# Optimization experiments

Hardware: AMD Instinct MI355X
Metric: run time of the kernel (lower is better)

Reference implementation:

```python
import jax, jax.numpy as jnp
import numpy as np
from jax import lax

V = 50000          # vocab
E = 64             # embedding_dim
B = 64             # batch
SEQ = 1024         # sentence length
NC = 6             # num_classes
L = 4              # num_layers (total conv layers)
KTOP = 4
NF = [10, 14, 18, 22]          # num_filters per stage
KS = [7, 5, 5, 3]              # kernel sizes
ROWS = [E // 2**i for i in range(5)]   # [64,32,16,8,4]
GROUPS = ROWS[:4]              # conv_i groups = rows[i-1]
# dynamic k-max schedule: k_l = max(k_top, ceil((L-l)/L * SEQ)) for l=1,2,3; last pool uses k_top
KPOOL = [max(KTOP, int(np.ceil((L - l) / L * SEQ))) for l in (1, 2, 3)] + [KTOP]  # [768,512,256,4]


def _uniform(key, shape, fan):
    s = 1.0 / np.sqrt(fan)
    return jax.random.uniform(key, shape, jnp.float32, -s, s)


def setup_inputs() -> dict:
    key = jax.random.key(0)
    ks = jax.random.split(key, 16)
    tokens = jax.random.randint(ks[0], (B, SEQ), 0, V)
    emb = jax.random.normal(ks[1], (V, E), jnp.float32)
    inp = {"tokens": tokens, "emb": emb}
    # conv weights: OIH layout, I = in_channels / groups = num_filters[i-1] (or 1 for conv1)
    in_pg = [1, NF[0], NF[1], NF[2]]
    out_ch = [NF[i] * ROWS[i] for i in range(4)]   # [640,448,288,176]
    for i in range(4):
        fan = in_pg[i] * KS[i]
        inp[f"w{i+1}"] = _uniform(ks[2 + 2 * i], (out_ch[i], in_pg[i], KS[i]), fan)
        inp[f"b{i+1}"] = _uniform(ks[3 + 2 * i], (out_ch[i],), fan)
    fc_in = ROWS[4] * NF[3] * KTOP   # 4*22*4 = 352
    inp["fcw"] = _uniform(ks[10], (NC, fc_in), fc_in)
    inp["fcb"] = _uniform(ks[11], (NC,), fc_in)
    return inp


def _fold(x, nf):
    # channel index c = row*nf + filt; sum adjacent rows pairwise (Fold(2,2))
    b, d, s = x.shape
    r = d // nf
    return x.reshape(b, r // 2, 2, nf, s).sum(axis=2).reshape(b, d // 2, s)


def _kmax(x, k):
    # top-k along seq axis, preserving original temporal order
    _, idx = lax.top_k(x, k)
    idx = jnp.sort(idx, axis=-1)
    return jnp.take_along_axis(x, idx, axis=-1)


def reference(tokens, emb, w1, b1, w2, b2, w3, b3, w4, b4, fcw, fcb):
    x = emb[tokens]                 # (B, S, E)
    x = x.transpose(0, 2, 1)        # (B, E, S)
    ws, bs = (w1, w2, w3, w4), (b1, b2, b3, b4)
    for i in range(4):
        pad = KS[i] - 1             # 'wide' convolution
        x = lax.conv_general_dilated(
            x, ws[i], (1,), [(pad, pad)],
            dimension_numbers=("NCH", "OIH", "NCH"),
            feature_group_count=GROUPS[i],
        ) + bs[i][None, :, None]
        x = _fold(x, NF[i])
        x = _kmax(x, KPOOL[i])
        x = jnp.tanh(x)
    # dropout is identity in eval mode
    x = x.reshape(x.shape[0], -1)   # (B, 352)
    return x @ fcw.T + fcb
```

## Files before the change

### kernel.cpp

```cpp
#include <hip/hip_runtime.h>
#include <hip/hip_bf16.h>
#include <math.h>


#if defined(__has_builtin)
#if __has_builtin(__builtin_amdgcn_ballot_w64)
#define BALLOT64(expr) __builtin_amdgcn_ballot_w64(expr)
#endif
#endif
#ifndef BALLOT64
#define BALLOT64(expr) __ballot(expr)
#endif

__device__ __forceinline__ unsigned f2ord(float f) {
    unsigned u = __float_as_uint(f);
    return (u & 0x80000000u) ? ~u : (u | 0x80000000u);
}
__device__ __forceinline__ float ord2f(unsigned key) {
    unsigned u = (key & 0x80000000u) ? (key & 0x7fffffffu) : ~key;
    return __uint_as_float(u);
}
__device__ __forceinline__ float tanh_fast(float x) {
    float e = __expf(2.f * x);
    return 1.f - 2.f * __builtin_amdgcn_rcpf(e + 1.f);
}
__device__ __forceinline__ int mbcnt64(unsigned long long m) {
    return __builtin_amdgcn_mbcnt_hi((unsigned)(m >> 32),
           __builtin_amdgcn_mbcnt_lo((unsigned)m, 0u));
}

template<int CH>
__device__ __forceinline__ int count_ge(const unsigned* keys, unsigned t) {
    int c = 0;
    #pragma unroll
    for (int i = 0; i < CH; ++i)
        c += __popcll(BALLOT64((keys[i] >= t)));
    return c;
}

template<int CH>
__device__ __forceinline__ void select_finish(const unsigned* keys, unsigned T,
                                              int k, float* stage,
                                              float* __restrict__ out)
{
    int g = 0, e = 0;
    #pragma unroll
    for (int i = 0; i < CH; ++i) { g += (keys[i] > T); e += (keys[i] == T); }

    int gtBefore = 0, eqBefore = 0, totG = 0;
    #pragma unroll
    for (int b = 0; b < 5; ++b) {
        unsigned long long mg = BALLOT64((((g >> b) & 1) != 0));
        unsigned long long me = BALLOT64((((e >> b) & 1) != 0));
        gtBefore += mbcnt64(mg) << b;
        eqBefore += mbcnt64(me) << b;
        totG     += __popcll(mg) << b;
    }
    const int needTies = k - totG;

    int gRun = 0, eRun = 0;
    #pragma unroll
    for (int i = 0; i < CH; ++i) {
        const unsigned key = keys[i];
        const bool isG = key > T;
        const bool isE = key == T;
        const int eIdx = eqBefore + eRun;
        const int dst = gtBefore + gRun + min(eIdx, needTies);
        if (isG || (isE && eIdx < needTies))
            stage[dst] = tanh_fast(ord2f(key));
        gRun += isG; eRun += isE;
    }
    const int lane = threadIdx.x & 63;
    float4* o4 = (float4*)out;
    const float4* s4 = (const float4*)stage;
    for (int i = lane; i < (k >> 2); i += 64)
        o4[i] = s4[i];
}

template<int N, int CH, int RADIX>
__device__ void wave_selectN(const unsigned (*keys)[CH], int k, float* stage,
                             float* const* outs)
{
    unsigned p[N];
    int above[N], buck[N];
    #pragma unroll
    for (int n = 0; n < N; ++n) { p[n] = 0u; above[n] = 0; buck[n] = 64 * CH; }

    unsigned doneMask = 0;
    const unsigned allDone = (1u << N) - 1u;

    if (RADIX == 4) {
        #pragma unroll 1
        for (int pos = 15; pos >= 0; --pos) {
            #pragma unroll
            for (int n = 0; n < N; ++n) {
                if (!((doneMask >> n) & 1u)) {
                    const int sh = 2 * pos;
                    const unsigned t1 = p[n] | (1u << sh);
                    const unsigned t2 = p[n] | (2u << sh);
                    const unsigned t3 = p[n] | (3u << sh);
                    const int c1 = count_ge<CH>(keys[n], t1);
                    const int c2 = count_ge<CH>(keys[n], t2);
                    const int c3 = count_ge<CH>(keys[n], t3);
                    const int rem = k - above[n];
                    if (c3 - above[n] >= rem) {
                        p[n] = t3; buck[n] = c3 - above[n];
                    } else if (c2 - above[n] >= rem) {
                        p[n] = t2; buck[n] = c2 - c3; above[n] = c3;
                    } else if (c1 - above[n] >= rem) {
                        p[n] = t1; buck[n] = c1 - c2; above[n] = c2;
                    } else {
                        buck[n] -= (c1 - above[n]); above[n] = c1;
                    }
                    if (buck[n] == k - above[n]) doneMask |= (1u << n);
                }
            }
            if (doneMask == allDone) break;
        }
    } else {
        #pragma unroll 1
        for (int pos = 31; pos >= 0; --pos) {
            #pragma unroll
            for (int n = 0; n < N; ++n) {
                if (!((doneMask >> n) & 1u)) {
                    const unsigned t = p[n] | (1u << pos);
                    const int c = count_ge<CH>(keys[n], t);
                    const int inb = c - above[n];
                    const int rem = k - above[n];
                    if (inb >= rem) { p[n] = t; buck[n] = inb; }
                    else            { above[n] += inb; buck[n] -= inb; }
                    if (buck[n] == k - above[n]) doneMask |= (1u << n);
                }
            }
            if (doneMask == allDone) break;
        }
    }
    #pragma unroll
    for (int n = 0; n < N; ++n)
        select_finish<CH>(keys[n], p[n], k, stage, outs[n]);
}

__global__ __launch_bounds__(128) void layer1_fused(
    const int* __restrict__ tokens, const float* __restrict__ emb,
    const float* __restrict__ W1, const float* __restrict__ B1,
    float* __restrict__ Z1)
{
    const int j = blockIdx.x;
    const int b = blockIdx.y;
    const int t = threadIdx.x;
    const int w = t >> 6;
    const int lane = t & 63;

    __shared__ float xr[2][1100];
    __shared__ __align__(16) float stagebuf[2][768];

    const float2* emb2 = (const float2*)emb;
    for (int i = t; i < 1100; i += 128) {
        int s = i - 6;
        float a = 0.f, c = 0.f;
        if (s >= 0 && s < 1024) {
            int tok = tokens[b * 1024 + s];
            float2 v = emb2[(size_t)tok * 32 + j];
            a = v.x; c = v.y;
        }
        xr[0][i] = a;
        xr[1][i] = c;
    }
    __syncthreads();

    const int beg = lane * 17;

    float x0[23], x1[23];
    #pragma unroll
    for (int i = 0; i < 23; ++i) { x0[i] = xr[0][beg + i]; x1[i] = xr[1][beg + i]; }

    unsigned keys[5][17];
    float* outs[5];
    const size_t orow = (size_t)b * 320 + (size_t)j * 10;

    #pragma unroll
    for (int q = 0; q < 5; ++q) {
        const int f = 5 * w + q;
        float wa[7], wb[7];
        #pragma unroll
        for (int k2 = 0; k2 < 7; ++k2) {
            wa[k2] = W1[(2 * j * 10 + f) * 7 + k2];
            wb[k2] = W1[((2 * j + 1) * 10 + f) * 7 + k2];
        }
        const float bias = B1[2 * j * 10 + f] + B1[(2 * j + 1) * 10 + f];
        #pragma unroll
        for (int i = 0; i < 17; ++i) {
            float acc = bias;
            #pragma unroll
            for (int k2 = 0; k2 < 7; ++k2)
                acc += x0[i + k2] * wa[k2] + x1[i + k2] * wb[k2];
            keys[q][i] = (beg + i < 1030) ? f2ord(acc) : 0u;
        }
        outs[q] = Z1 + (orow + f) * 768;
    }
    wave_selectN<5, 17, 4>(keys, 768, stagebuf[w], outs);
}

template <int IPG, int NF, int K, int SIN, int SOUT, int KSEL, int NW, int CH,
          int PHASES>
__global__ __launch_bounds__(NW * 64) void conv_fold_select_kernel(
    const float* __restrict__ X, const float* __restrict__ W,
    const float* __restrict__ Bias, float* __restrict__ Z,
    int Cin, int Cfold)
{
    static_assert(NF == 2 * NW, "2 filters per wave");
    static_assert(64 * CH >= SOUT, "chunk covers row");
    constexpr int W2 = 64 * CH + K - 1;
    constexpr int RS = 2 * IPG / PHASES;

    const int t = threadIdx.x;
    const int j = blockIdx.x;
    const int b = blockIdx.y;
    const int wav = t >> 6, lane = t & 63;

    __shared__ float xs[RS][W2];
    __shared__ __align__(16) float stagebuf[NW][KSEL];

    const float* Xb = X + ((size_t)b * Cin + (size_t)(2 * j) * IPG) * SIN;

    const int f0 = __builtin_amdgcn_readfirstlane(2 * wav);
    float acc0[CH], acc1[CH];
    {
        float bias0 = Bias[2 * j * NF + f0]     + Bias[(2 * j + 1) * NF + f0];
        float bias1 = Bias[2 * j * NF + f0 + 1] + Bias[(2 * j + 1) * NF + f0 + 1];
        #pragma unroll
        for (int i = 0; i < CH; ++i) { acc0[i] = bias0; acc1[i] = bias1; }
    }
    const int base = lane * CH;

    #pragma unroll 1
    for (int ph = 0; ph < PHASES; ++ph) {
        if (ph) __syncthreads();
        for (int idx = t; idx < RS * W2; idx += NW * 64) {
            int r = idx / W2, p = idx - r * W2;
            int sg = p - (K - 1);
            int gr = ph * RS + r;
            xs[r][p] = (sg >= 0 && sg < SIN) ? Xb[(size_t)gr * SIN + sg] : 0.f;
        }
        __syncthreads();

        int h = (ph * RS) / IPG, c = (ph * RS) % IPG;
        #pragma unroll 1
        for (int r = 0; r < RS; ++r) {
            float win[CH + K - 1];
            #pragma unroll
            for (int p = 0; p < CH + K - 1; ++p)
                win[p] = xs[r][base + p];
            const float* Wp = W + ((size_t)((2 * j + h) * NF + f0) * IPG + c) * K;
            #pragma unroll
            for (int k2 = 0; k2 < K; ++k2) {
                const float w0 = Wp[k2];
                const float w1 = Wp[(size_t)IPG * K + k2];
                #pragma unroll
                for (int i = 0; i < CH; ++i) {
                    acc0[i] = fmaf(win[i + k2], w0, acc0[i]);
                    acc1[i] = fmaf(win[i + k2], w1, acc1[i]);
                }
            }
            if (++c == IPG) { c = 0; ++h; }
        }
    }

    unsigned keys[2][CH];
    #pragma unroll
    for (int i = 0; i < CH; ++i) {
        keys[0][i] = (base + i < SOUT) ? f2ord(acc0[i]) : 0u;
        keys[1][i] = (base + i < SOUT) ? f2ord(acc1[i]) : 0u;
    }
    const size_t orow = (size_t)b * Cfold + (size_t)j * NF;
    float* outs[2] = { Z + (orow + f0) * (size_t)KSEL,
                       Z + (orow + f0 + 1) * (size_t)KSEL };
    wave_selectN<2, CH, 2>(keys, KSEL, stagebuf[wav], outs);
}

__global__ __launch_bounds__(192) void fc_kernel(
    const float* __restrict__ Z, const float* __restrict__ Wf,
    const float* __restrict__ bf, float* __restrict__ out)
{
    int g = blockIdx.x * blockDim.x + threadIdx.x;
    if (g >= 64 * 6) return;
    int b = g / 6, c = g % 6;
    float acc = bf[c];
    const float* zr = Z + b * 352;
    const float* wr = Wf + c * 352;
    for (int i = 0; i < 352; ++i) acc += zr[i] * wr[i];
    out[g] = acc;
}

extern "C" void kernel_launch(void* const* d_in, const int* in_sizes, int n_in,
                              void* d_out, int out_size, void* d_ws, size_t ws_size,
                              hipStream_t stream)
{
    const int*   tokens = (const int*)  d_in[0];
    const float* emb    = (const float*)d_in[1];
    const float* w1     = (const float*)d_in[2];
    const float* b1     = (const float*)d_in[3];
    const float* w2     = (const float*)d_in[4];
    const float* b2     = (const float*)d_in[5];
    const float* w3     = (const float*)d_in[6];
    const float* b3     = (const float*)d_in[7];
    const float* w4     = (const float*)d_in[8];
    const float* b4     = (const float*)d_in[9];
    const float* fcw    = (const float*)d_in[10];
    const float* fcb    = (const float*)d_in[11];
    float* out = (float*)d_out;
    float* ws  = (float*)d_ws;

    float* Z1 = ws;
    float* Z2 = ws + 15728640;
    float* Z3 = ws;
    float* Z4 = ws + 2359296;

    layer1_fused<<<dim3(32, 64), 128, 0, stream>>>(tokens, emb, w1, b1, Z1);

    conv_fold_select_kernel<10, 14, 5, 768, 772, 512, 7, 13, 2>
        <<<dim3(16, 64), 7 * 64, 0, stream>>>(Z1, w2, b2, Z2, 320, 224);

    conv_fold_select_kernel<14, 18, 5, 512, 516, 256, 9, 9, 1>
        <<<dim3(8, 64), 9 * 64, 0, stream>>>(Z2, w3, b3, Z3, 224, 144);

    conv_fold_select_kernel<18, 22, 3, 256, 258, 4, 11, 5, 1>
        <<<dim3(4, 64), 11 * 64, 0, stream>>>(Z3, w4, b4, Z4, 144, 88);

    fc_kernel<<<2, 192, 0, stream>>>(Z4, fcw, fcb, out);
}
```

Measured before the change: 345.8 us.

## Fuse layers 1-2 and 3-4 into kernels keeping intermediates in LDS

Merges the layer-1 conv+fold+k-max with the layer-2 conv so Z1 stays in shared memory and never goes to global memory. Likewise merges layers 3 and 4 so Z3 lives in LDS, cutting five launches to three. The selection routine now takes per-row stage pointers and can skip the global write. In exchange, blocks get larger with heavy LDS use (about 85KB for l12), which lowers occupancy. The l34 kernel also has only 256 blocks, and layer-3 work runs on 9 of its 11 waves.

```diff
diff --git a/kernel.cpp b/kernel.cpp
--- a/kernel.cpp
+++ b/kernel.cpp
@@ -70,16 +70,18 @@
             stage[dst] = tanh_fast(ord2f(key));
         gRun += isG; eRun += isE;
     }
-    const int lane = threadIdx.x & 63;
-    float4* o4 = (float4*)out;
-    const float4* s4 = (const float4*)stage;
-    for (int i = lane; i < (k >> 2); i += 64)
-        o4[i] = s4[i];
+    if (out) {
+        const int lane = threadIdx.x & 63;
+        float4* o4 = (float4*)out;
+        const float4* s4 = (const float4*)stage;
+        for (int i = lane; i < (k >> 2); i += 64)
+            o4[i] = s4[i];
+    }
 }
 
 template<int N, int CH, int RADIX>
-__device__ void wave_selectN(const unsigned (*keys)[CH], int k, float* stage,
-                             float* const* outs)
+__device__ void wave_selectN(const unsigned (*keys)[CH], int k,
+                             float* const* stages, float* const* outs)
 {
     unsigned p[N];
     int above[N], buck[N];
@@ -137,145 +139,246 @@
     }
     #pragma unroll
     for (int n = 0; n < N; ++n)
-        select_finish<CH>(keys[n], p[n], k, stage, outs[n]);
-}
-
-__global__ __launch_bounds__(128) void layer1_fused(
+        select_finish<CH>(keys[n], p[n], k, stages[n], outs[n]);
+}
+
+#define L1RW 1100
+#define Z1W  840
+
+__global__ __launch_bounds__(640) void l12_fused(
     const int* __restrict__ tokens, const float* __restrict__ emb,
     const float* __restrict__ W1, const float* __restrict__ B1,
-    float* __restrict__ Z1)
-{
-    const int j = blockIdx.x;
-    const int b = blockIdx.y;
-    const int t = threadIdx.x;
-    const int w = t >> 6;
+    const float* __restrict__ W2, const float* __restrict__ B2,
+    float* __restrict__ Z2)
+{
+    const int j2 = blockIdx.x;
+    const int b  = blockIdx.y;
+    const int t  = threadIdx.x;
+    const int wav  = __builtin_amdgcn_readfirstlane(t >> 6);
     const int lane = t & 63;
 
-    __shared__ float xr[2][1100];
-    __shared__ __align__(16) float stagebuf[2][768];
-
-    const float2* emb2 = (const float2*)emb;
-    for (int i = t; i < 1100; i += 128) {
+    __shared__ __align__(16) float xr[4][L1RW];
+    __shared__ __align__(16) float z1[20][Z1W];
+
+    const float4* emb4 = (const float4*)emb;
+    for (int i = t; i < L1RW; i += 640) {
         int s = i - 6;
-        float a = 0.f, c = 0.f;
+        float4 v = make_float4(0.f, 0.f, 0.f, 0.f);
         if (s >= 0 && s < 1024) {
             int tok = tokens[b * 1024 + s];
-            float2 v = emb2[(size_t)tok * 32 + j];
-            a = v.x; c = v.y;
-        }
-        xr[0][i] = a;
-        xr[1][i] = c;
+            v = emb4[(size_t)tok * 16 + j2];
+        }
+        xr[0][i] = v.x; xr[1][i] = v.y; xr[2][i] = v.z; xr[3][i] = v.w;
+    }
+    {
+        const int PERROW = 4 + (Z1W - 772);
+        for (int i = t; i < 20 * PERROW; i += 640) {
+            int r = i / PERROW, p = i - r * PERROW;
+            z1[r][(p < 4) ? p : (772 + p - 4)] = 0.f;
+        }
     }
     __syncthreads();
 
-    const int beg = lane * 17;
-
-    float x0[23], x1[23];
-    #pragma unroll
-    for (int i = 0; i < 23; ++i) { x0[i] = xr[0][beg + i]; x1[i] = xr[1][beg + i]; }
-
-    unsigned keys[5][17];
-    float* outs[5];
-    const size_t orow = (size_t)b * 320 + (size_t)j * 10;
-
-    #pragma unroll
-    for (int q = 0; q < 5; ++q) {
-        const int f = 5 * w + q;
-        float wa[7], wb[7];
+    {
+        const int jj = wav / 5;
+        const int q  = wav % 5;
+        const int jg = 2 * j2 + jj;
+        const int beg = lane * 17;
+
+        float x0[23], x1[23];
         #pragma unroll
-        for (int k2 = 0; k2 < 7; ++k2) {
-            wa[k2] = W1[(2 * j * 10 + f) * 7 + k2];
-            wb[k2] = W1[((2 * j + 1) * 10 + f) * 7 + k2];
-        }
-        const float bias = B1[2 * j * 10 + f] + B1[(2 * j + 1) * 10 + f];
+        for (int i = 0; i < 23; ++i) {
+            x0[i] = xr[2 * jj][beg + i];
+            x1[i] = xr[2 * jj + 1][beg + i];
+        }
+
+        unsigned keys[2][17];
+        float* stages[2];
+        float* outs[2] = { nullptr, nullptr };
         #pragma unroll
-        for (int i = 0; i < 17; ++i) {
-            float acc = bias;
-            #pragma unroll
-            for (int k2 = 0; k2 < 7; ++k2)
-                acc += x0[i + k2] * wa[k2] + x1[i + k2] * wb[k2];
-            keys[q][i] = (beg + i < 1030) ? f2ord(acc) : 0u;
-        }
-        outs[q] = Z1 + (orow + f) * 768;
-    }
-    wave_selectN<5, 17, 4>(keys, 768, stagebuf[w], outs);
-}
-
-template <int IPG, int NF, int K, int SIN, int SOUT, int KSEL, int NW, int CH,
-          int PHASES>
-__global__ __launch_bounds__(NW * 64) void conv_fold_select_kernel(
-    const float* __restrict__ X, const float* __restrict__ W,
-    const float* __restrict__ Bias, float* __restrict__ Z,
-    int Cin, int Cfold)
-{
-    static_assert(NF == 2 * NW, "2 filters per wave");
-    static_assert(64 * CH >= SOUT, "chunk covers row");
-    constexpr int W2 = 64 * CH + K - 1;
-    constexpr int RS = 2 * IPG / PHASES;
-
-    const int t = threadIdx.x;
-    const int j = blockIdx.x;
-    const int b = blockIdx.y;
-    const int wav = t >> 6, lane = t & 63;
-
-    __shared__ float xs[RS][W2];
-    __shared__ __align__(16) float stagebuf[NW][KSEL];
-
-    const float* Xb = X + ((size_t)b * Cin + (size_t)(2 * j) * IPG) * SIN;
-
-    const int f0 = __builtin_amdgcn_readfirstlane(2 * wav);
-    float acc0[CH], acc1[CH];
-    {
-        float bias0 = Bias[2 * j * NF + f0]     + Bias[(2 * j + 1) * NF + f0];
-        float bias1 = Bias[2 * j * NF + f0 + 1] + Bias[(2 * j + 1) * NF + f0 + 1];
-        #pragma unroll
-        for (int i = 0; i < CH; ++i) { acc0[i] = bias0; acc1[i] = bias1; }
-    }
-    const int base = lane * CH;
-
-    #pragma unroll 1
-    for (int ph = 0; ph < PHASES; ++ph) {
-        if (ph) __syncthreads();
-        for (int idx = t; idx < RS * W2; idx += NW * 64) {
-            int r = idx / W2, p = idx - r * W2;
-            int sg = p - (K - 1);
-            int gr = ph * RS + r;
-            xs[r][p] = (sg >= 0 && sg < SIN) ? Xb[(size_t)gr * SIN + sg] : 0.f;
-        }
-        __syncthreads();
-
-        int h = (ph * RS) / IPG, c = (ph * RS) % IPG;
+        for (int n = 0; n < 2; ++n) {
+            const int f = q + 5 * n;
+            float wa[7], wb[7];
+            #pragma unroll
+            for (int k2 = 0; k2 < 7; ++k2) {
+                wa[k2] = W1[(2 * jg * 10 + f) * 7 + k2];
+                wb[k2] = W1[((2 * jg + 1) * 10 + f) * 7 + k2];
+            }
+            const float bias = B1[2 * jg * 10 + f] + B1[(2 * jg + 1) * 10 + f];
+            #pragma unroll
+            for (int i = 0; i < 17; ++i) {
+                float acc = bias;
+                #pragma unroll
+                for (int k2 = 0; k2 < 7; ++k2)
+                    acc += x0[i + k2] * wa[k2] + x1[i + k2] * wb[k2];
+                keys[n][i] = (beg + i < 1030) ? f2ord(acc) : 0u;
+            }
+            stages[n] = &z1[jj * 10 + f][4];
+        }
+        wave_selectN<2, 17, 4>(keys, 768, stages, outs);
+    }
+    __syncthreads();
+
+    if (wav < 7) {
+        const int f0 = 2 * wav;
+        const int base = lane * 13;
+        float acc0[13], acc1[13];
+        {
+            const float b0 = B2[2 * j2 * 14 + f0]     + B2[(2 * j2 + 1) * 14 + f0];
+            const float b1 = B2[2 * j2 * 14 + f0 + 1] + B2[(2 * j2 + 1) * 14 + f0 + 1];
+            #pragma unroll
+            for (int i = 0; i < 13; ++i) { acc0[i] = b0; acc1[i] = b1; }
+        }
         #pragma unroll 1
-        for (int r = 0; r < RS; ++r) {
-            float win[CH + K - 1];
-            #pragma unroll
-            for (int p = 0; p < CH + K - 1; ++p)
-                win[p] = xs[r][base + p];
-            const float* Wp = W + ((size_t)((2 * j + h) * NF + f0) * IPG + c) * K;
-            #pragma unroll
-            for (int k2 = 0; k2 < K; ++k2) {
+        for (int r = 0; r < 20; ++r) {
+            const int h = r / 10, c = r - 10 * (r / 10);
+            float win[17];
+            #pragma unroll
+            for (int p = 0; p < 17; ++p) win[p] = z1[r][base + p];
+            const float* Wp = W2 + ((size_t)((2 * j2 + h) * 14 + f0) * 10 + c) * 5;
+            #pragma unroll
+            for (int k2 = 0; k2 < 5; ++k2) {
                 const float w0 = Wp[k2];
-                const float w1 = Wp[(size_t)IPG * K + k2];
-                #pragma unroll
-                for (int i = 0; i < CH; ++i) {
+                const float w1 = Wp[50 + k2];
+                #pragma unroll
+                for (int i = 0; i < 13; ++i) {
                     acc0[i] = fmaf(win[i + k2], w0, acc0[i]);
                     acc1[i] = fmaf(win[i + k2], w1, acc1[i]);
                 }
             }
-            if (++c == IPG) { c = 0; ++h; }
-        }
-    }
-
-    unsigned keys[2][CH];
-    #pragma unroll
-    for (int i = 0; i < CH; ++i) {
-        keys[0][i] = (base + i < SOUT) ? f2ord(acc0[i]) : 0u;
-        keys[1][i] = (base + i < SOUT) ? f2ord(acc1[i]) : 0u;
-    }
-    const size_t orow = (size_t)b * Cfold + (size_t)j * NF;
-    float* outs[2] = { Z + (orow + f0) * (size_t)KSEL,
-                       Z + (orow + f0 + 1) * (size_t)KSEL };
-    wave_selectN<2, CH, 2>(keys, KSEL, stagebuf[wav], outs);
+        }
+        unsigned keys[2][13];
+        #pragma unroll
+        for (int i = 0; i < 13; ++i) {
+            keys[0][i] = (base + i < 772) ? f2ord(acc0[i]) : 0u;
+            keys[1][i] = (base + i < 772) ? f2ord(acc1[i]) : 0u;
+        }
+        float* st = &xr[0][0] + wav * 512;
+        float* stages[2] = { st, st };
+        const size_t orow = (size_t)b * 224 + (size_t)j2 * 14;
+        float* outs[2] = { Z2 + (orow + f0) * 512, Z2 + (orow + f0 + 1) * 512 };
+        wave_selectN<2, 13, 2>(keys, 512, stages, outs);
+    }
+}
+
+#define X2W 580
+#define Z3W 324
+
+__global__ __launch_bounds__(704) void l34_fused(
+    const float* __restrict__ Z2, const float* __restrict__ W3,
+    const float* __restrict__ B3, const float* __restrict__ W4,
+    const float* __restrict__ B4, float* __restrict__ Z4)
+{
+    const int j4 = blockIdx.x;
+    const int b  = blockIdx.y;
+    const int t  = threadIdx.x;
+    const int wav  = __builtin_amdgcn_readfirstlane(t >> 6);
+    const int lane = t & 63;
+
+    __shared__ __align__(16) float x2[28][X2W];
+    __shared__ __align__(16) float z3[36][Z3W];
+
+    {
+        const int PERROW = 2 + (Z3W - 258);
+        for (int i = t; i < 36 * PERROW; i += 704) {
+            int r = i / PERROW, p = i - r * PERROW;
+            z3[r][(p < 2) ? p : (258 + p - 2)] = 0.f;
+        }
+    }
+
+    #pragma unroll 1
+    for (int ph = 0; ph < 2; ++ph) {
+        if (ph) __syncthreads();
+        const float* Zb = Z2 + ((size_t)b * 224 + (size_t)(4 * j4 + 2 * ph) * 14) * 512;
+        for (int idx = t; idx < 28 * X2W; idx += 704) {
+            int r = idx / X2W, p = idx - r * X2W;
+            int sg = p - 4;
+            x2[r][p] = (sg >= 0 && sg < 512) ? Zb[(size_t)r * 512 + sg] : 0.f;
+        }
+        __syncthreads();
+
+        if (wav < 9) {
+            const int f0 = 2 * wav;
+            const int j3 = 2 * j4 + ph;
+            const int base = lane * 9;
+            float acc0[9], acc1[9];
+            {
+                const float b0 = B3[2 * j3 * 18 + f0]     + B3[(2 * j3 + 1) * 18 + f0];
+                const float b1 = B3[2 * j3 * 18 + f0 + 1] + B3[(2 * j3 + 1) * 18 + f0 + 1];
+                #pragma unroll
+                for (int i = 0; i < 9; ++i) { acc0[i] = b0; acc1[i] = b1; }
+            }
+            #pragma unroll 1
+            for (int r = 0; r < 28; ++r) {
+                const int h = r / 14, c = r - 14 * (r / 14);
+                float win[13];
+                #pragma unroll
+                for (int p = 0; p < 13; ++p) win[p] = x2[r][base + p];
+                const float* Wp = W3 + ((size_t)((2 * j3 + h) * 18 + f0) * 14 + c) * 5;
+                #pragma unroll
+                for (int k2 = 0; k2 < 5; ++k2) {
+                    const float w0 = Wp[k2];
+                    const float w1 = Wp[70 + k2];
+                    #pragma unroll
+                    for (int i = 0; i < 9; ++i) {
+                        acc0[i] = fmaf(win[i + k2], w0, acc0[i]);
+                        acc1[i] = fmaf(win[i + k2], w1, acc1[i]);
+                    }
+                }
+            }
+            unsigned keys[2][9];
+            #pragma unroll
+            for (int i = 0; i < 9; ++i) {
+                keys[0][i] = (base + i < 516) ? f2ord(acc0[i]) : 0u;
+                keys[1][i] = (base + i < 516) ? f2ord(acc1[i]) : 0u;
+            }
+            float* stages[2] = { &z3[18 * ph + f0][2], &z3[18 * ph + f0 + 1][2] };
+            float* outs[2] = { nullptr, nullptr };
+            wave_selectN<2, 9, 2>(keys, 256, stages, outs);
+        }
+    }
+    __syncthreads();
+
+    {
+        const int f0 = 2 * wav;
+        const int base = lane * 5;
+        float acc0[5], acc1[5];
+        {
+            const float b0 = B4[2 * j4 * 22 + f0]     + B4[(2 * j4 + 1) * 22 + f0];
+            const float b1 = B4[2 * j4 * 22 + f0 + 1] + B4[(2 * j4 + 1) * 22 + f0 + 1];
+            #pragma unroll
+            for (int i = 0; i < 5; ++i) { acc0[i] = b0; acc1[i] = b1; }
+        }
+        #pragma unroll 1
+        for (int r = 0; r < 36; ++r) {
+            const int h = r / 18, c = r - 18 * (r / 18);
+            float win[7];
+            #pragma unroll
+            for (int p = 0; p < 7; ++p) win[p] = z3[r][base + p];
+            const float* Wp = W4 + ((size_t)((2 * j4 + h) * 22 + f0) * 18 + c) * 3;
+            #pragma unroll
+            for (int k2 = 0; k2 < 3; ++k2) {
+                const float w0 = Wp[k2];
+                const float w1 = Wp[54 + k2];
+                #pragma unroll
+                for (int i = 0; i < 5; ++i) {
+                    acc0[i] = fmaf(win[i + k2], w0, acc0[i]);
+                    acc1[i] = fmaf(win[i + k2], w1, acc1[i]);
+                }
+            }
+        }
+        unsigned keys[2][5];
+        #pragma unroll
+        for (int i = 0; i < 5; ++i) {
+            keys[0][i] = (base + i < 258) ? f2ord(acc0[i]) : 0u;
+            keys[1][i] = (base + i < 258) ? f2ord(acc1[i]) : 0u;
+        }
+        float* st = &x2[0][0] + wav * 4;
+        float* stages[2] = { st, st };
+        const size_t orow = (size_t)b * 88 + (size_t)j4 * 22;
+        float* outs[2] = { Z4 + (orow + f0) * 4, Z4 + (orow + f0 + 1) * 4 };
+        wave_selectN<2, 5, 2>(keys, 4, stages, outs);
+    }
 }
 
 __global__ __launch_bounds__(192) void fc_kernel(
@@ -311,21 +414,10 @@
     float* out = (float*)d_out;
     float* ws  = (float*)d_ws;
 
-    float* Z1 = ws;
-    float* Z2 = ws + 15728640;
-    float* Z3 = ws;
-    float* Z4 = ws + 2359296;
-
-    layer1_fused<<<dim3(32, 64), 128, 0, stream>>>(tokens, emb, w1, b1, Z1);
-
-    conv_fold_select_kernel<10, 14, 5, 768, 772, 512, 7, 13, 2>
-        <<<dim3(16, 64), 7 * 64, 0, stream>>>(Z1, w2, b2, Z2, 320, 224);
-
-    conv_fold_select_kernel<14, 18, 5, 512, 516, 256, 9, 9, 1>
-        <<<dim3(8, 64), 9 * 64, 0, stream>>>(Z2, w3, b3, Z3, 224, 144);
-
-    conv_fold_select_kernel<18, 22, 3, 256, 258, 4, 11, 5, 1>
-        <<<dim3(4, 64), 11 * 64, 0, stream>>>(Z3, w4, b4, Z4, 144, 88);
-
+    float* Z2 = ws;
+    float* Z4 = ws + 7340032;
+
+    l12_fused<<<dim3(16, 64), 640, 0, stream>>>(tokens, emb, w1, b1, w2, b2, Z2);
+    l34_fused<<<dim3(4, 64), 704, 0, stream>>>(Z2, w3, b3, w4, b4, Z4);
     fc_kernel<<<2, 192, 0, stream>>>(Z4, fcw, fcb, out);
 }
```

Result: slower. 357.6 us (+3.4%).

## Fuse layer1 and layer2 via shared-memory Z1, add radix-8 select and packed FMA

Applied to the files above, without the earlier changes.

Layer 1 conv+fold+kmax and layer 2 conv now run in one kernel. Each block builds the 20 folded layer-1 rows it needs in LDS, so the large Z1 intermediate is never written to or read back from global memory. The layer-1 top-k switches to a radix-8 threshold search to cut the number of passes, and the convolutions use 2-wide vector FMAs so the packed-FP32 instructions can be used. Risks include high LDS use per block (about 81KB), which limits occupancy, plus larger 640-thread blocks and more compare work per radix pass.

```diff
diff --git a/kernel.cpp b/kernel.cpp
--- a/kernel.cpp
+++ b/kernel.cpp
@@ -2,6 +2,8 @@
 #include <hip/hip_bf16.h>
 #include <math.h>
 
+
+typedef float v2f __attribute__((ext_vector_type(2)));
 
 #if defined(__has_builtin)
 #if __has_builtin(__builtin_amdgcn_ballot_w64)
@@ -70,16 +72,18 @@
             stage[dst] = tanh_fast(ord2f(key));
         gRun += isG; eRun += isE;
     }
-    const int lane = threadIdx.x & 63;
-    float4* o4 = (float4*)out;
-    const float4* s4 = (const float4*)stage;
-    for (int i = lane; i < (k >> 2); i += 64)
-        o4[i] = s4[i];
+    if (out) {
+        const int lane = threadIdx.x & 63;
+        float4* o4 = (float4*)out;
+        const float4* s4 = (const float4*)stage;
+        for (int i = lane; i < (k >> 2); i += 64)
+            o4[i] = s4[i];
+    }
 }
 
 template<int N, int CH, int RADIX>
-__device__ void wave_selectN(const unsigned (*keys)[CH], int k, float* stage,
-                             float* const* outs)
+__device__ void wave_selectN(const unsigned (*keys)[CH], int k,
+                             float* const* stages, float* const* outs)
 {
     unsigned p[N];
     int above[N], buck[N];
@@ -89,29 +93,42 @@
     unsigned doneMask = 0;
     const unsigned allDone = (1u << N) - 1u;
 
-    if (RADIX == 4) {
+    if (RADIX == 8) {
+        #pragma unroll
+        for (int n = 0; n < N; ++n) {
+            const int c1 = count_ge<CH>(keys[n], 1u << 30);
+            const int c2 = count_ge<CH>(keys[n], 2u << 30);
+            const int c3 = count_ge<CH>(keys[n], 3u << 30);
+            const int rem = k;
+            if (c3 >= rem)      { p[n] = 3u << 30; buck[n] = c3; }
+            else if (c2 >= rem) { p[n] = 2u << 30; buck[n] = c2 - c3; above[n] = c3; }
+            else if (c1 >= rem) { p[n] = 1u << 30; buck[n] = c1 - c2; above[n] = c2; }
+            else                { buck[n] -= c1; above[n] = c1; }
+            if (buck[n] == k - above[n]) doneMask |= (1u << n);
+        }
         #pragma unroll 1
-        for (int pos = 15; pos >= 0; --pos) {
+        for (int pos = 9; pos >= 0; --pos) {
             #pragma unroll
             for (int n = 0; n < N; ++n) {
                 if (!((doneMask >> n) & 1u)) {
-                    const int sh = 2 * pos;
-                    const unsigned t1 = p[n] | (1u << sh);
-                    const unsigned t2 = p[n] | (2u << sh);
-                    const unsigned t3 = p[n] | (3u << sh);
-                    const int c1 = count_ge<CH>(keys[n], t1);
-                    const int c2 = count_ge<CH>(keys[n], t2);
-                    const int c3 = count_ge<CH>(keys[n], t3);
-                    const int rem = k - above[n];
-                    if (c3 - above[n] >= rem) {
-                        p[n] = t3; buck[n] = c3 - above[n];
-                    } else if (c2 - above[n] >= rem) {
-                        p[n] = t2; buck[n] = c2 - c3; above[n] = c3;
-                    } else if (c1 - above[n] >= rem) {
-                        p[n] = t1; buck[n] = c1 - c2; above[n] = c2;
-                    } else {
-                        buck[n] -= (c1 - above[n]); above[n] = c1;
-                    }
+                    const int sh = 3 * pos;
+                    const int c1 = count_ge<CH>(keys[n], p[n] | (1u << sh));
+                    const int c2 = count_ge<CH>(keys[n], p[n] | (2u << sh));
+                    const int c3 = count_ge<CH>(keys[n], p[n] | (3u << sh));
+                    const int c4 = count_ge<CH>(keys[n], p[n] | (4u << sh));
+                    const int c5 = count_ge<CH>(keys[n], p[n] | (5u << sh));
+                    const int c6 = count_ge<CH>(keys[n], p[n] | (6u << sh));
+                    const int c7 = count_ge<CH>(keys[n], p[n] | (7u << sh));
+                    const int ab = above[n];
+                    const int rem = k - ab;
+                    if      (c7 - ab >= rem) { p[n] |= 7u << sh; buck[n] = c7 - ab; }
+                    else if (c6 - ab >= rem) { p[n] |= 6u << sh; buck[n] = c6 - c7; above[n] = c7; }
+                    else if (c5 - ab >= rem) { p[n] |= 5u << sh; buck[n] = c5 - c6; above[n] = c6; }
+                    else if (c4 - ab >= rem) { p[n] |= 4u << sh; buck[n] = c4 - c5; above[n] = c5; }
+                    else if (c3 - ab >= rem) { p[n] |= 3u << sh; buck[n] = c3 - c4; above[n] = c4; }
+                    else if (c2 - ab >= rem) { p[n] |= 2u << sh; buck[n] = c2 - c3; above[n] = c3; }
+                    else if (c1 - ab >= rem) { p[n] |= 1u << sh; buck[n] = c1 - c2; above[n] = c2; }
+                    else                     { buck[n] -= (c1 - ab); above[n] = c1; }
                     if (buck[n] == k - above[n]) doneMask |= (1u << n);
                 }
             }
@@ -137,72 +154,135 @@
     }
     #pragma unroll
     for (int n = 0; n < N; ++n)
-        select_finish<CH>(keys[n], p[n], k, stage, outs[n]);
-}
-
-__global__ __launch_bounds__(128) void layer1_fused(
+        select_finish<CH>(keys[n], p[n], k, stages[n], outs[n]);
+}
+
+#define L1RW 1100
+#define Z1W  840
+
+__global__ __launch_bounds__(640) void l12_fused(
     const int* __restrict__ tokens, const float* __restrict__ emb,
     const float* __restrict__ W1, const float* __restrict__ B1,
-    float* __restrict__ Z1)
-{
-    const int j = blockIdx.x;
-    const int b = blockIdx.y;
-    const int t = threadIdx.x;
-    const int w = t >> 6;
+    const float* __restrict__ W2, const float* __restrict__ B2,
+    float* __restrict__ Z2)
+{
+    const int j2 = blockIdx.x;
+    const int b  = blockIdx.y;
+    const int t  = threadIdx.x;
+    const int wav  = __builtin_amdgcn_readfirstlane(t >> 6);
     const int lane = t & 63;
 
-    __shared__ float xr[2][1100];
-    __shared__ __align__(16) float stagebuf[2][768];
-
-    const float2* emb2 = (const float2*)emb;
-    for (int i = t; i < 1100; i += 128) {
+    __shared__ __align__(16) float xr[4][L1RW];
+    __shared__ __align__(16) float z1[20][Z1W];
+
+    const float4* emb4 = (const float4*)emb;
+    for (int i = t; i < L1RW; i += 640) {
         int s = i - 6;
-        float a = 0.f, c = 0.f;
+        float4 v = make_float4(0.f, 0.f, 0.f, 0.f);
         if (s >= 0 && s < 1024) {
             int tok = tokens[b * 1024 + s];
-            float2 v = emb2[(size_t)tok * 32 + j];
-            a = v.x; c = v.y;
-        }
-        xr[0][i] = a;
-        xr[1][i] = c;
+            v = emb4[(size_t)tok * 16 + j2];
+        }
+        xr[0][i] = v.x; xr[1][i] = v.y; xr[2][i] = v.z; xr[3][i] = v.w;
+    }
+    {
+        const int PERROW = 4 + (Z1W - 772);
+        for (int i = t; i < 20 * PERROW; i += 640) {
+            int r = i / PERROW, p = i - r * PERROW;
+            z1[r][(p < 4) ? p : (772 + p - 4)] = 0.f;
+        }
     }
     __syncthreads();
 
-    const int beg = lane * 17;
-
-    float x0[23], x1[23];
-    #pragma unroll
-    for (int i = 0; i < 23; ++i) { x0[i] = xr[0][beg + i]; x1[i] = xr[1][beg + i]; }
-
-    unsigned keys[5][17];
-    float* outs[5];
-    const size_t orow = (size_t)b * 320 + (size_t)j * 10;
-
-    #pragma unroll
-    for (int q = 0; q < 5; ++q) {
-        const int f = 5 * w + q;
-        float wa[7], wb[7];
+    {
+        const int jj = wav / 5;
+        const int q  = wav % 5;
+        const int jg = 2 * j2 + jj;
+        const int beg = lane * 17;
+
+        float x0[23], x1[23];
+        #pragma unroll
+        for (int i = 0; i < 23; ++i) {
+            x0[i] = xr[2 * jj][beg + i];
+            x1[i] = xr[2 * jj + 1][beg + i];
+        }
+
+        v2f vwa[7], vwb[7];
         #pragma unroll
         for (int k2 = 0; k2 < 7; ++k2) {
-            wa[k2] = W1[(2 * j * 10 + f) * 7 + k2];
-            wb[k2] = W1[((2 * j + 1) * 10 + f) * 7 + k2];
-        }
-        const float bias = B1[2 * j * 10 + f] + B1[(2 * j + 1) * 10 + f];
+            v2f a = { W1[(2 * jg * 10 + q) * 7 + k2],
+                      W1[(2 * jg * 10 + q + 5) * 7 + k2] };
+            v2f bb = { W1[((2 * jg + 1) * 10 + q) * 7 + k2],
+                       W1[((2 * jg + 1) * 10 + q + 5) * 7 + k2] };
+            vwa[k2] = a; vwb[k2] = bb;
+        }
+        v2f vbias = { B1[2 * jg * 10 + q]     + B1[(2 * jg + 1) * 10 + q],
+                      B1[2 * jg * 10 + q + 5] + B1[(2 * jg + 1) * 10 + q + 5] };
+
+        unsigned keys[2][17];
         #pragma unroll
         for (int i = 0; i < 17; ++i) {
-            float acc = bias;
-            #pragma unroll
-            for (int k2 = 0; k2 < 7; ++k2)
-                acc += x0[i + k2] * wa[k2] + x1[i + k2] * wb[k2];
-            keys[q][i] = (beg + i < 1030) ? f2ord(acc) : 0u;
-        }
-        outs[q] = Z1 + (orow + f) * 768;
-    }
-    wave_selectN<5, 17, 4>(keys, 768, stagebuf[w], outs);
-}
-
-template <int IPG, int NF, int K, int SIN, int SOUT, int KSEL, int NW, int CH,
-          int PHASES>
+            v2f acc = vbias;
+            #pragma unroll
+            for (int k2 = 0; k2 < 7; ++k2) {
+                v2f s0 = { x0[i + k2], x0[i + k2] };
+                v2f s1 = { x1[i + k2], x1[i + k2] };
+                acc = __builtin_elementwise_fma(s0, vwa[k2], acc);
+                acc = __builtin_elementwise_fma(s1, vwb[k2], acc);
+            }
+            const bool ok = (beg + i < 1030);
+            keys[0][i] = ok ? f2ord(acc.x) : 0u;
+            keys[1][i] = ok ? f2ord(acc.y) : 0u;
+        }
+        float* stages[2] = { &z1[jj * 10 + q][4], &z1[jj * 10 + q + 5][4] };
+        float* outs[2] = { nullptr, nullptr };
+        wave_selectN<2, 17, 8>(keys, 768, stages, outs);
+    }
+    __syncthreads();
+
+    if (wav < 7) {
+        const int f0 = 2 * wav;
+        const int base = lane * 13;
+        v2f vacc[13];
+        {
+            v2f vb = { B2[2 * j2 * 14 + f0]     + B2[(2 * j2 + 1) * 14 + f0],
+                       B2[2 * j2 * 14 + f0 + 1] + B2[(2 * j2 + 1) * 14 + f0 + 1] };
+            #pragma unroll
+            for (int i = 0; i < 13; ++i) vacc[i] = vb;
+        }
+        #pragma unroll 1
+        for (int r = 0; r < 20; ++r) {
+            const int h = r / 10, c = r - 10 * (r / 10);
+            float win[17];
+            #pragma unroll
+            for (int p = 0; p < 17; ++p) win[p] = z1[r][base + p];
+            const float* Wp = W2 + ((size_t)((2 * j2 + h) * 14 + f0) * 10 + c) * 5;
+            #pragma unroll
+            for (int k2 = 0; k2 < 5; ++k2) {
+                v2f vw = { Wp[k2], Wp[50 + k2] };
+                #pragma unroll
+                for (int i = 0; i < 13; ++i) {
+                    v2f s = { win[i + k2], win[i + k2] };
+                    vacc[i] = __builtin_elementwise_fma(s, vw, vacc[i]);
+                }
+            }
+        }
+        unsigned keys[2][13];
+        #pragma unroll
+        for (int i = 0; i < 13; ++i) {
+            const bool ok = (base + i < 772);
+            keys[0][i] = ok ? f2ord(vacc[i].x) : 0u;
+            keys[1][i] = ok ? f2ord(vacc[i].y) : 0u;
+        }
+        float* st = &xr[0][0] + wav * 512;
+        float* stages[2] = { st, st };
+        const size_t orow = (size_t)b * 224 + (size_t)j2 * 14;
+        float* outs[2] = { Z2 + (orow + f0) * 512, Z2 + (orow + f0 + 1) * 512 };
+        wave_selectN<2, 13, 2>(keys, 512, stages, outs);
+    }
+}
+
+template <int IPG, int NF, int K, int SIN, int SOUT, int KSEL, int NW, int CH>
 __global__ __launch_bounds__(NW * 64) void conv_fold_select_kernel(
     const float* __restrict__ X, const float* __restrict__ W,
     const float* __restrict__ Bias, float* __restrict__ Z,
@@ -211,71 +291,65 @@
     static_assert(NF == 2 * NW, "2 filters per wave");
     static_assert(64 * CH >= SOUT, "chunk covers row");
     constexpr int W2 = 64 * CH + K - 1;
-    constexpr int RS = 2 * IPG / PHASES;
 
     const int t = threadIdx.x;
     const int j = blockIdx.x;
     const int b = blockIdx.y;
-    const int wav = t >> 6, lane = t & 63;
-
-    __shared__ float xs[RS][W2];
+    const int wav = __builtin_amdgcn_readfirstlane(t >> 6);
+    const int lane = t & 63;
+
+    __shared__ float xs[2 * IPG][W2];
     __shared__ __align__(16) float stagebuf[NW][KSEL];
 
     const float* Xb = X + ((size_t)b * Cin + (size_t)(2 * j) * IPG) * SIN;
-
-    const int f0 = __builtin_amdgcn_readfirstlane(2 * wav);
-    float acc0[CH], acc1[CH];
+    for (int idx = t; idx < 2 * IPG * W2; idx += NW * 64) {
+        int r = idx / W2, p = idx - r * W2;
+        int sg = p - (K - 1);
+        xs[r][p] = (sg >= 0 && sg < SIN) ? Xb[(size_t)r * SIN + sg] : 0.f;
+    }
+    __syncthreads();
+
+    const int f0 = 2 * wav;
+    v2f vacc[CH];
     {
-        float bias0 = Bias[2 * j * NF + f0]     + Bias[(2 * j + 1) * NF + f0];
-        float bias1 = Bias[2 * j * NF + f0 + 1] + Bias[(2 * j + 1) * NF + f0 + 1];
-        #pragma unroll
-        for (int i = 0; i < CH; ++i) { acc0[i] = bias0; acc1[i] = bias1; }
+        v2f vb = { Bias[2 * j * NF + f0]     + Bias[(2 * j + 1) * NF + f0],
+                   Bias[2 * j * NF + f0 + 1] + Bias[(2 * j + 1) * NF + f0 + 1] };
+        #pragma unroll
+        for (int i = 0; i < CH; ++i) vacc[i] = vb;
     }
     const int base = lane * CH;
 
     #pragma unroll 1
-    for (int ph = 0; ph < PHASES; ++ph) {
-        if (ph) __syncthreads();
-        for (int idx = t; idx < RS * W2; idx += NW * 64) {
-            int r = idx / W2, p = idx - r * W2;
-            int sg = p - (K - 1);
-            int gr = ph * RS + r;
-            xs[r][p] = (sg >= 0 && sg < SIN) ? Xb[(size_t)gr * SIN + sg] : 0.f;
-        }
-        __syncthreads();
-
-        int h = (ph * RS) / IPG, c = (ph * RS) % IPG;
-        #pragma unroll 1
-        for (int r = 0; r < RS; ++r) {
-            float win[CH + K - 1];
-            #pragma unroll
-            for (int p = 0; p < CH + K - 1; ++p)
-                win[p] = xs[r][base + p];
-            const float* Wp = W + ((size_t)((2 * j + h) * NF + f0) * IPG + c) * K;
-            #pragma unroll
-            for (int k2 = 0; k2 < K; ++k2) {
-                const float w0 = Wp[k2];
-                const float w1 = Wp[(size_t)IPG * K + k2];
-                #pragma unroll
-                for (int i = 0; i < CH; ++i) {
-                    acc0[i] = fmaf(win[i + k2], w0, acc0[i]);
-                    acc1[i] = fmaf(win[i + k2], w1, acc1[i]);
-                }
+    for (int r = 0; r < 2 * IPG; ++r) {
+        const int h = r / IPG, c = r - IPG * (r / IPG);
+        float win[CH + K - 1];
+        #pragma unroll
+        for (int p = 0; p < CH + K - 1; ++p)
+            win[p] = xs[r][base + p];
+        const float* Wp = W + ((size_t)((2 * j + h) * NF + f0) * IPG + c) * K;
+        #pragma unroll
+        for (int k2 = 0; k2 < K; ++k2) {
+            v2f vw = { Wp[k2], Wp[(size_t)IPG * K + k2] };
+            #pragma unroll
+            for (int i = 0; i < CH; ++i) {
+                v2f s = { win[i + k2], win[i + k2] };
+                vacc[i] = __builtin_elementwise_fma(s, vw, vacc[i]);
             }
-            if (++c == IPG) { c = 0; ++h; }
         }
     }
 
     unsigned keys[2][CH];
     #pragma unroll
     for (int i = 0; i < CH; ++i) {
-        keys[0][i] = (base + i < SOUT) ? f2ord(acc0[i]) : 0u;
-        keys[1][i] = (base + i < SOUT) ? f2ord(acc1[i]) : 0u;
+        const bool ok = (base + i < SOUT);
+        keys[0][i] = ok ? f2ord(vacc[i].x) : 0u;
+        keys[1][i] = ok ? f2ord(vacc[i].y) : 0u;
     }
     const size_t orow = (size_t)b * Cfold + (size_t)j * NF;
+    float* stages[2] = { stagebuf[wav], stagebuf[wav] };
     float* outs[2] = { Z + (orow + f0) * (size_t)KSEL,
                        Z + (orow + f0 + 1) * (size_t)KSEL };
-    wave_selectN<2, CH, 2>(keys, KSEL, stagebuf[wav], outs);
+    wave_selectN<2, CH, 2>(keys, KSEL, stages, outs);
 }
 
 __global__ __launch_bounds__(192) void fc_kernel(
@@ -311,20 +385,16 @@
     float* out = (float*)d_out;
     float* ws  = (float*)d_ws;
 
-    float* Z1 = ws;
-    float* Z2 = ws + 15728640;
-    float* Z3 = ws;
-    float* Z4 = ws + 2359296;
-
-    layer1_fused<<<dim3(32, 64), 128, 0, stream>>>(tokens, emb, w1, b1, Z1);
-
-    conv_fold_select_kernel<10, 14, 5, 768, 772, 512, 7, 13, 2>
-        <<<dim3(16, 64), 7 * 64, 0, stream>>>(Z1, w2, b2, Z2, 320, 224);
-
-    conv_fold_select_kernel<14, 18, 5, 512, 516, 256, 9, 9, 1>
+    float* Z2 = ws;
+    float* Z3 = ws + 7340032;
+    float* Z4 = ws + 9699328;
+
+    l12_fused<<<dim3(16, 64), 640, 0, stream>>>(tokens, emb, w1, b1, w2, b2, Z2);
+
+    conv_fold_select_kernel<14, 18, 5, 512, 516, 256, 9, 9>
         <<<dim3(8, 64), 9 * 64, 0, stream>>>(Z2, w3, b3, Z3, 224, 144);
 
-    conv_fold_select_kernel<18, 22, 3, 256, 258, 4, 11, 5, 1>
+    conv_fold_select_kernel<18, 22, 3, 256, 258, 4, 11, 5>
         <<<dim3(4, 64), 11 * 64, 0, stream>>>(Z3, w4, b4, Z4, 144, 88);
 
     fc_kernel<<<2, 192, 0, stream>>>(Z4, fcw, fcb, out);
```

Result: slower. 420.8 us (+21.7%).
